# Kernel optimization log

Measured on AMD Instinct MI355X. Metric: run time of the kernel, lower is better.

## Reference

```python
import jax, jax.numpy as jnp
import numpy as np
from jax import lax

B, T, E, D, A, C, FILT = 32, 1600, 1024, 1024, 512, 10, 100
SCALING = 2.0


def setup_inputs() -> dict:
    key = jax.random.key(0)
    ks = jax.random.split(key, 14)
    enc_hs_pad = jax.random.normal(ks[0], (B, T, E), dtype=jnp.float32)
    # lengths in [T//2, T] so every row has valid positions
    enc_hs_len = jax.random.randint(ks[1], (B,), T // 2, T + 1, dtype=jnp.int32)
    dec_z = jax.random.normal(ks[2], (B, D), dtype=jnp.float32)
    # previous attention weights: uniform over valid frames, normalized
    valid = (jnp.arange(T)[None, :] < enc_hs_len[:, None]).astype(jnp.float32)
    raw = jax.random.uniform(ks[3], (B, T), dtype=jnp.float32) * valid
    att_prev = raw / jnp.sum(raw, axis=1, keepdims=True)
    att_h = 0.1 * jax.random.normal(ks[4], (B, A), dtype=jnp.float32)
    att_c = 0.1 * jax.random.normal(ks[5], (B, A), dtype=jnp.float32)
    W_enc = jax.random.normal(ks[6], (A, E), dtype=jnp.float32) / np.sqrt(E)
    b_enc = jax.random.normal(ks[7], (A,), dtype=jnp.float32) * 0.01
    W_dec = jax.random.normal(ks[8], (A, D), dtype=jnp.float32) / np.sqrt(D)
    conv_w = jax.random.normal(ks[9], (C, 1, 2 * FILT + 1), dtype=jnp.float32) / np.sqrt(2 * FILT + 1)
    W_ih = jax.random.normal(ks[10], (4 * A, C), dtype=jnp.float32) / np.sqrt(C)
    W_hh = jax.random.normal(ks[11], (4 * A, A), dtype=jnp.float32) / np.sqrt(A)
    W_g = jax.random.normal(ks[12], (A,), dtype=jnp.float32) / np.sqrt(A)
    b_g = jnp.zeros((1,), dtype=jnp.float32)
    return {"enc_hs_pad": enc_hs_pad, "enc_hs_len": enc_hs_len, "dec_z": dec_z,
            "att_prev": att_prev, "att_h": att_h, "att_c": att_c,
            "W_enc": W_enc, "b_enc": b_enc, "W_dec": W_dec, "conv_w": conv_w,
            "W_ih": W_ih, "W_hh": W_hh, "W_g": W_g, "b_g": b_g}


def reference(enc_hs_pad, enc_hs_len, dec_z, att_prev, att_h, att_c,
              W_enc, b_enc, W_dec, conv_w, W_ih, W_hh, W_g, b_g):
    t_len = enc_hs_pad.shape[1]
    filts = (conv_w.shape[-1] - 1) // 2

    # precompute encoder projection (B, T, A)
    pre_enc = jnp.einsum('bte,ae->bta', enc_hs_pad, W_enc) + b_enc

    # location conv on previous attention: (B,1,T) -> (B,C,T), relu, global max-pool over T
    att_conv = lax.conv_general_dilated(att_prev[:, None, :], conv_w,
                                        window_strides=(1,), padding=[(filts, filts)],
                                        dimension_numbers=('NCH', 'OIH', 'NCH'))
    att_feat = jnp.max(jax.nn.relu(att_conv), axis=-1)  # (B, C)

    # LSTMCell (no bias), pytorch gate order i, f, g, o
    gates = att_feat @ W_ih.T + att_h @ W_hh.T  # (B, 4A)
    i, f, g, o = jnp.split(gates, 4, axis=-1)
    c_new = jax.nn.sigmoid(f) * att_c + jax.nn.sigmoid(i) * jnp.tanh(g)
    h_new = jax.nn.sigmoid(o) * jnp.tanh(c_new)  # (B, A)

    dec_proj = dec_z @ W_dec.T  # (B, A)
    # scores (B, T)
    e = jnp.tanh(h_new[:, None, :] + pre_enc + dec_proj[:, None, :]) @ W_g + b_g

    mask = jnp.arange(t_len)[None, :] >= enc_hs_len[:, None]  # True = pad
    e = jnp.where(mask, jnp.finfo(e.dtype).min, e)
    w = jax.nn.softmax(SCALING * e, axis=1)  # (B, T)

    ctx = jnp.einsum('bt,bte->be', w, enc_hs_pad)  # (B, E)
    return ctx, w, h_new, c_new
```

## Files before the change

### kernel.cpp

```cpp
#include <hip/hip_runtime.h>

#define BB 32
#define TT 1600
#define EE 1024
#define DD 1024
#define AA 512
#define CC 10
#define KW 201

typedef __attribute__((ext_vector_type(8))) short short8;
typedef __attribute__((ext_vector_type(4))) float f32x4;

__device__ __forceinline__ unsigned short f2bf(float f) {
    unsigned int u = __float_as_uint(f);
    unsigned int r = (u + 0x7fffu + ((u >> 16) & 1u)) >> 16;
    return (unsigned short)r;
}
__device__ __forceinline__ float sigm(float x) { return 1.f / (1.f + expf(-x)); }

#define AF_OFF    0
#define GATES_OFF 320
#define DEC_OFF   65856
#define R_OFF     82240
#define E_OFF     98624
#define WBF_OFF   149824

#define CTX_OFF 0
#define W_OFF   32768
#define H_OFF   83968
#define C_OFF   100352

__global__ void zero_kernel(float* out, float* af) {
    int i = blockIdx.x * 256 + threadIdx.x;
    if (i < 32768) out[CTX_OFF + i] = 0.f;
    else if (i < 32768 + 320) af[i - 32768] = 0.f;
}

__global__ void wconv_kernel(const float* __restrict__ W_enc, unsigned short* __restrict__ Wbf) {
    int i = blockIdx.x * 256 + threadIdx.x;
    float4 v = reinterpret_cast<const float4*>(W_enc)[i];
    ushort4 p;
    p.x = f2bf(v.x); p.y = f2bf(v.y); p.z = f2bf(v.z); p.w = f2bf(v.w);
    reinterpret_cast<ushort4*>(Wbf)[i] = p;
}

__global__ void conv_kernel(const float* __restrict__ att_prev,
                            const float* __restrict__ conv_w,
                            unsigned int* __restrict__ af) {
    int b = blockIdx.x, c = blockIdx.y, seg = blockIdx.z;
    int ts = seg * 400;
    __shared__ float x[600];
    __shared__ float red[256];
    int tid = threadIdx.x;
    const float* xp = att_prev + b * TT;
    for (int i = tid; i < 600; i += 256) {
        int g = ts - 100 + i;
        x[i] = (g >= 0 && g < TT) ? xp[g] : 0.f;
    }
    __syncthreads();
    const float* wrow = conv_w + c * KW;
    float mx = 0.f;
    for (int tt = tid; tt < 400; tt += 256) {
        float s = 0.f;
        #pragma unroll 4
        for (int k = 0; k < KW; ++k) s += wrow[k] * x[tt + k];
        mx = fmaxf(mx, s);
    }
    red[tid] = mx; __syncthreads();
    for (int s = 128; s > 0; s >>= 1) {
        if (tid < s) red[tid] = fmaxf(red[tid], red[tid + s]);
        __syncthreads();
    }
    if (tid == 0) atomicMax(&af[b * CC + c], __float_as_uint(red[0]));
}

__global__ void small_gemm_kernel(const float* __restrict__ af,
                                  const float* __restrict__ att_h,
                                  const float* __restrict__ dec_z,
                                  const float* __restrict__ W_ih,
                                  const float* __restrict__ W_hh,
                                  const float* __restrict__ W_dec,
                                  float* __restrict__ gates,
                                  float* __restrict__ dec_proj) {
    int tid = threadIdx.x;
    int b = tid & 31, jl = tid >> 5;
    int j = blockIdx.x * 8 + jl;
    if (j < 2048) {
        float s = 0.f;
        #pragma unroll
        for (int k = 0; k < 10; ++k) s += af[b * 10 + k] * W_ih[j * 10 + k];
        const float4* hh4 = reinterpret_cast<const float4*>(W_hh + (size_t)j * 512);
        const float4* h4  = reinterpret_cast<const float4*>(att_h + b * 512);
        #pragma unroll 4
        for (int k = 0; k < 128; ++k) {
            float4 a = h4[k], w = hh4[k];
            s += a.x * w.x + a.y * w.y + a.z * w.z + a.w * w.w;
        }
        gates[b * 2048 + j] = s;
    } else {
        int a = j - 2048;
        const float4* wd4 = reinterpret_cast<const float4*>(W_dec + (size_t)a * 1024);
        const float4* z4  = reinterpret_cast<const float4*>(dec_z + b * 1024);
        float s = 0.f;
        #pragma unroll 4
        for (int k = 0; k < 256; ++k) {
            float4 a4 = z4[k], w = wd4[k];
            s += a4.x * w.x + a4.y * w.y + a4.z * w.z + a4.w * w.w;
        }
        dec_proj[b * 512 + a] = s;
    }
}

__global__ void lstm_kernel(const float* __restrict__ gates,
                            const float* __restrict__ att_c,
                            const float* __restrict__ dec_proj,
                            float* __restrict__ out,
                            float* __restrict__ r) {
    int idx = blockIdx.x * 256 + threadIdx.x;
    int b = idx >> 9, a = idx & 511;
    const float* g = gates + b * 2048;
    float ig = g[a], fg = g[512 + a], gg = g[1024 + a], og = g[1536 + a];
    float cn = sigm(fg) * att_c[idx] + sigm(ig) * tanhf(gg);
    float hn = sigm(og) * tanhf(cn);
    out[H_OFF + idx] = hn;
    out[C_OFF + idx] = cn;
    r[idx] = hn + dec_proj[idx];
}

__global__ void __launch_bounds__(256, 2)
score_gemm_kernel(const float* __restrict__ enc,
                  const unsigned short* __restrict__ Wbf,
                  const float* __restrict__ b_enc,
                  const float* __restrict__ r_ws,
                  const float* __restrict__ W_g,
                  const float* __restrict__ b_g,
                  float* __restrict__ e_out) {
    __shared__ short As[64 * 40];
    __shared__ short Bs[512 * 40];
    __shared__ float e_sm[64];

    int tid = threadIdx.x;
    int lane = tid & 63, wv = tid >> 6;
    int col = lane & 15, quad = lane >> 4;
    int m0 = blockIdx.x * 64;
    int b = blockIdx.x / 25;

    if (tid < 64) e_sm[tid] = 0.f;

    f32x4 acc[4][8];
    #pragma unroll
    for (int mt = 0; mt < 4; ++mt)
        #pragma unroll
        for (int nt = 0; nt < 8; ++nt)
            acc[mt][nt] = (f32x4){0.f, 0.f, 0.f, 0.f};

    for (int k0 = 0; k0 < 1024; k0 += 32) {
        __syncthreads();
        #pragma unroll
        for (int s = 0; s < 2; ++s) {
            int i = tid + s * 256;
            int row = i >> 3, kq = i & 7;
            float4 v = *reinterpret_cast<const float4*>(
                enc + (size_t)(m0 + row) * 1024 + k0 + kq * 4);
            ushort4 p;
            p.x = f2bf(v.x); p.y = f2bf(v.y); p.z = f2bf(v.z); p.w = f2bf(v.w);
            *reinterpret_cast<ushort4*>(&As[row * 40 + kq * 4]) = p;
        }
        #pragma unroll
        for (int s = 0; s < 8; ++s) {
            int i = tid + s * 256;
            int row = i >> 2, ko = (i & 3) * 8;
            int4 v = *reinterpret_cast<const int4*>(Wbf + (size_t)row * 1024 + k0 + ko);
            *reinterpret_cast<int4*>(&Bs[row * 40 + ko]) = v;
        }
        __syncthreads();

        short8 a_frag[4];
        #pragma unroll
        for (int mt = 0; mt < 4; ++mt)
            a_frag[mt] = *reinterpret_cast<const short8*>(&As[(mt * 16 + col) * 40 + quad * 8]);
        #pragma unroll
        for (int nt = 0; nt < 8; ++nt) {
            short8 b_frag = *reinterpret_cast<const short8*>(
                &Bs[(wv * 128 + nt * 16 + col) * 40 + quad * 8]);
            #pragma unroll
            for (int mt = 0; mt < 4; ++mt)
                acc[mt][nt] = __builtin_amdgcn_mfma_f32_16x16x32_bf16(
                    a_frag[mt], b_frag, acc[mt][nt], 0, 0, 0);
        }
    }

    float bn[8], rn[8], wg[8];
    #pragma unroll
    for (int nt = 0; nt < 8; ++nt) {
        int n = wv * 128 + nt * 16 + col;
        bn[nt] = b_enc[n];
        rn[nt] = r_ws[b * 512 + n];
        wg[nt] = W_g[n];
    }
    #pragma unroll
    for (int mt = 0; mt < 4; ++mt) {
        #pragma unroll
        for (int reg = 0; reg < 4; ++reg) {
            float p = 0.f;
            #pragma unroll
            for (int nt = 0; nt < 8; ++nt)
                p += wg[nt] * tanhf(acc[mt][nt][reg] + bn[nt] + rn[nt]);
            p += __shfl_xor(p, 1);
            p += __shfl_xor(p, 2);
            p += __shfl_xor(p, 4);
            p += __shfl_xor(p, 8);
            if (col == 0) atomicAdd(&e_sm[mt * 16 + quad * 4 + reg], p);
        }
    }
    __syncthreads();
    if (tid < 64) e_out[m0 + tid] = e_sm[tid] + b_g[0];
}

__global__ void softmax_kernel(const float* __restrict__ e_ws,
                               const int* __restrict__ lens,
                               float* __restrict__ w_out) {
    int b = blockIdx.x, tid = threadIdx.x;
    int len = lens[b];
    const float* e = e_ws + b * TT;
    __shared__ float red[256];
    float mx = -3.4e38f;
    for (int t = tid; t < len; t += 256) mx = fmaxf(mx, e[t]);
    red[tid] = mx; __syncthreads();
    for (int s = 128; s > 0; s >>= 1) {
        if (tid < s) red[tid] = fmaxf(red[tid], red[tid + s]);
        __syncthreads();
    }
    mx = red[0]; __syncthreads();
    float sum = 0.f;
    for (int t = tid; t < len; t += 256) sum += expf(2.f * (e[t] - mx));
    red[tid] = sum; __syncthreads();
    for (int s = 128; s > 0; s >>= 1) {
        if (tid < s) red[tid] += red[tid + s];
        __syncthreads();
    }
    float inv = 1.f / red[0];
    for (int t = tid; t < TT; t += 256)
        w_out[b * TT + t] = (t < len) ? expf(2.f * (e[t] - mx)) * inv : 0.f;
}

__global__ void ctx_kernel(const float* __restrict__ enc,
                           const float* __restrict__ w,
                           float* __restrict__ ctx) {
    int b = blockIdx.x, seg = blockIdx.y;
    int t0 = seg * 200;
    const float* wrow = w + b * TT;
    float4 acc = {0.f, 0.f, 0.f, 0.f};
    for (int t = t0; t < t0 + 200; ++t) {
        float wv = wrow[t];
        if (wv == 0.f) continue;
        float4 v = *reinterpret_cast<const float4*>(
            enc + (size_t)(b * TT + t) * 1024 + threadIdx.x * 4);
        acc.x += wv * v.x; acc.y += wv * v.y; acc.z += wv * v.z; acc.w += wv * v.w;
    }
    float* dst = ctx + b * 1024 + threadIdx.x * 4;
    atomicAdd(dst + 0, acc.x);
    atomicAdd(dst + 1, acc.y);
    atomicAdd(dst + 2, acc.z);
    atomicAdd(dst + 3, acc.w);
}

extern "C" void kernel_launch(void* const* d_in, const int* in_sizes, int n_in,
                              void* d_out, int out_size, void* d_ws, size_t ws_size,
                              hipStream_t stream) {
    const float* enc      = (const float*)d_in[0];
    const int*   lens     = (const int*)d_in[1];
    const float* dec_z    = (const float*)d_in[2];
    const float* att_prev = (const float*)d_in[3];
    const float* att_h    = (const float*)d_in[4];
    const float* att_c    = (const float*)d_in[5];
    const float* W_enc    = (const float*)d_in[6];
    const float* b_enc    = (const float*)d_in[7];
    const float* W_dec    = (const float*)d_in[8];
    const float* conv_w   = (const float*)d_in[9];
    const float* W_ih     = (const float*)d_in[10];
    const float* W_hh     = (const float*)d_in[11];
    const float* W_g      = (const float*)d_in[12];
    const float* b_g      = (const float*)d_in[13];

    float* out = (float*)d_out;
    float* ws  = (float*)d_ws;
    float* af        = ws + AF_OFF;
    float* gates     = ws + GATES_OFF;
    float* dec_proj  = ws + DEC_OFF;
    float* r_ws      = ws + R_OFF;
    float* e_ws      = ws + E_OFF;
    unsigned short* Wbf = (unsigned short*)(ws + WBF_OFF);

    zero_kernel<<<130, 256, 0, stream>>>(out, af);
    wconv_kernel<<<512, 256, 0, stream>>>(W_enc, Wbf);
    conv_kernel<<<dim3(BB, CC, 4), 256, 0, stream>>>(att_prev, conv_w, (unsigned int*)af);
    small_gemm_kernel<<<320, 256, 0, stream>>>(af, att_h, dec_z, W_ih, W_hh, W_dec,
                                               gates, dec_proj);
    lstm_kernel<<<64, 256, 0, stream>>>(gates, att_c, dec_proj, out, r_ws);
    score_gemm_kernel<<<800, 256, 0, stream>>>(enc, Wbf, b_enc, r_ws, W_g, b_g, e_ws);
    softmax_kernel<<<BB, 256, 0, stream>>>(e_ws, lens, out + W_OFF);
    ctx_kernel<<<dim3(BB, 8), 256, 0, stream>>>(enc, out + W_OFF, out + CTX_OFF);
}
```

Baseline: 559.3 us.

## Retile score GEMM to 128x128 blocks with direct-to-LDS weight loads

```diff
diff --git a/kernel.cpp b/kernel.cpp
--- a/kernel.cpp
+++ b/kernel.cpp
@@ -1,9 +1,9 @@
 #include <hip/hip_runtime.h>
+#include <hip/hip_bf16.h>
 
 #define BB 32
 #define TT 1600
 #define EE 1024
-#define DD 1024
 #define AA 512
 #define CC 10
 #define KW 201
@@ -11,12 +11,21 @@
 typedef __attribute__((ext_vector_type(8))) short short8;
 typedef __attribute__((ext_vector_type(4))) float f32x4;
 
-__device__ __forceinline__ unsigned short f2bf(float f) {
-    unsigned int u = __float_as_uint(f);
-    unsigned int r = (u + 0x7fffu + ((u >> 16) & 1u)) >> 16;
-    return (unsigned short)r;
-}
 __device__ __forceinline__ float sigm(float x) { return 1.f / (1.f + expf(-x)); }
+
+__device__ __forceinline__ unsigned int cvt2(float a, float b) {
+    float2 f2; f2.x = a; f2.y = b;
+    __hip_bfloat162 h = __float22bfloat162_rn(f2);
+    unsigned int r;
+    __builtin_memcpy(&r, &h, 4);
+    return r;
+}
+
+__device__ __forceinline__ void gl_lds16(const void* g, void* l) {
+    __builtin_amdgcn_global_load_lds(
+        (const __attribute__((address_space(1))) unsigned int*)g,
+        (__attribute__((address_space(3))) unsigned int*)l, 16, 0, 0);
+}
 
 #define AF_OFF    0
 #define GATES_OFF 320
@@ -30,18 +39,20 @@
 #define H_OFF   83968
 #define C_OFF   100352
 
-__global__ void zero_kernel(float* out, float* af) {
+__global__ void zero_kernel(float* out, float* af, float* e_ws) {
     int i = blockIdx.x * 256 + threadIdx.x;
     if (i < 32768) out[CTX_OFF + i] = 0.f;
-    else if (i < 32768 + 320) af[i - 32768] = 0.f;
+    else if (i < 33088) af[i - 32768] = 0.f;
+    else if (i < 84288) e_ws[i - 33088] = 0.f;
 }
 
 __global__ void wconv_kernel(const float* __restrict__ W_enc, unsigned short* __restrict__ Wbf) {
     int i = blockIdx.x * 256 + threadIdx.x;
     float4 v = reinterpret_cast<const float4*>(W_enc)[i];
-    ushort4 p;
-    p.x = f2bf(v.x); p.y = f2bf(v.y); p.z = f2bf(v.z); p.w = f2bf(v.w);
-    reinterpret_cast<ushort4*>(Wbf)[i] = p;
+    uint2 p;
+    p.x = cvt2(v.x, v.y);
+    p.y = cvt2(v.z, v.w);
+    reinterpret_cast<uint2*>(Wbf)[i] = p;
 }
 
 __global__ void conv_kernel(const float* __restrict__ att_prev,
@@ -50,6 +61,7 @@
     int b = blockIdx.x, c = blockIdx.y, seg = blockIdx.z;
     int ts = seg * 400;
     __shared__ float x[600];
+    __shared__ float wsm[KW];
     __shared__ float red[256];
     int tid = threadIdx.x;
     const float* xp = att_prev + b * TT;
@@ -57,13 +69,13 @@
         int g = ts - 100 + i;
         x[i] = (g >= 0 && g < TT) ? xp[g] : 0.f;
     }
+    if (tid < KW) wsm[tid] = conv_w[c * KW + tid];
     __syncthreads();
-    const float* wrow = conv_w + c * KW;
     float mx = 0.f;
     for (int tt = tid; tt < 400; tt += 256) {
         float s = 0.f;
         #pragma unroll 4
-        for (int k = 0; k < KW; ++k) s += wrow[k] * x[tt + k];
+        for (int k = 0; k < KW; ++k) s += wsm[k] * x[tt + k];
         mx = fmaxf(mx, s);
     }
     red[tid] = mx; __syncthreads();
@@ -133,56 +145,58 @@
                   const float* __restrict__ b_enc,
                   const float* __restrict__ r_ws,
                   const float* __restrict__ W_g,
-                  const float* __restrict__ b_g,
-                  float* __restrict__ e_out) {
-    __shared__ short As[64 * 40];
-    __shared__ short Bs[512 * 40];
-    __shared__ float e_sm[64];
+                  float* __restrict__ e_ws) {
+    __shared__ __align__(16) short As[128 * 32];
+    __shared__ __align__(16) short Bs[128 * 32];
 
     int tid = threadIdx.x;
     int lane = tid & 63, wv = tid >> 6;
     int col = lane & 15, quad = lane >> 4;
-    int m0 = blockIdx.x * 64;
-    int b = blockIdx.x / 25;
-
-    if (tid < 64) e_sm[tid] = 0.f;
-
-    f32x4 acc[4][8];
+    int wm = wv >> 1, wn = wv & 1;
+    int n0 = blockIdx.x * 128;
+    int m0 = blockIdx.y * 128;
+
+    int arow = tid >> 1, ahalf = (tid & 1) * 16;
+    const float* abase = enc + (size_t)(m0 + arow) * EE + ahalf;
+
+    f32x4 acc[4][4];
     #pragma unroll
     for (int mt = 0; mt < 4; ++mt)
         #pragma unroll
-        for (int nt = 0; nt < 8; ++nt)
+        for (int nt = 0; nt < 4; ++nt)
             acc[mt][nt] = (f32x4){0.f, 0.f, 0.f, 0.f};
 
-    for (int k0 = 0; k0 < 1024; k0 += 32) {
-        __syncthreads();
-        #pragma unroll
-        for (int s = 0; s < 2; ++s) {
-            int i = tid + s * 256;
-            int row = i >> 3, kq = i & 7;
-            float4 v = *reinterpret_cast<const float4*>(
-                enc + (size_t)(m0 + row) * 1024 + k0 + kq * 4);
-            ushort4 p;
-            p.x = f2bf(v.x); p.y = f2bf(v.y); p.z = f2bf(v.z); p.w = f2bf(v.w);
-            *reinterpret_cast<ushort4*>(&As[row * 40 + kq * 4]) = p;
-        }
-        #pragma unroll
-        for (int s = 0; s < 8; ++s) {
-            int i = tid + s * 256;
-            int row = i >> 2, ko = (i & 3) * 8;
-            int4 v = *reinterpret_cast<const int4*>(Wbf + (size_t)row * 1024 + k0 + ko);
-            *reinterpret_cast<int4*>(&Bs[row * 40 + ko]) = v;
-        }
+    for (int k0 = 0; k0 < EE; k0 += 32) {
+        const float4* ag = reinterpret_cast<const float4*>(abase + k0);
+        float4 v0 = ag[0], v1 = ag[1], v2 = ag[2], v3 = ag[3];
+
+        __syncthreads();
+
+        {
+            int c = tid;
+            gl_lds16(Wbf + (size_t)(n0 + (c >> 2)) * EE + k0 + (c & 3) * 8, Bs + c * 8);
+            c = tid + 256;
+            gl_lds16(Wbf + (size_t)(n0 + (c >> 2)) * EE + k0 + (c & 3) * 8, Bs + c * 8);
+        }
+        int4 st0, st1;
+        st0.x = cvt2(v0.x, v0.y); st0.y = cvt2(v0.z, v0.w);
+        st0.z = cvt2(v1.x, v1.y); st0.w = cvt2(v1.z, v1.w);
+        st1.x = cvt2(v2.x, v2.y); st1.y = cvt2(v2.z, v2.w);
+        st1.z = cvt2(v3.x, v3.y); st1.w = cvt2(v3.z, v3.w);
+        *reinterpret_cast<int4*>(&As[arow * 32 + ahalf]) = st0;
+        *reinterpret_cast<int4*>(&As[arow * 32 + ahalf + 8]) = st1;
+
         __syncthreads();
 
         short8 a_frag[4];
         #pragma unroll
         for (int mt = 0; mt < 4; ++mt)
-            a_frag[mt] = *reinterpret_cast<const short8*>(&As[(mt * 16 + col) * 40 + quad * 8]);
-        #pragma unroll
-        for (int nt = 0; nt < 8; ++nt) {
+            a_frag[mt] = *reinterpret_cast<const short8*>(
+                &As[(wm * 64 + mt * 16 + col) * 32 + quad * 8]);
+        #pragma unroll
+        for (int nt = 0; nt < 4; ++nt) {
             short8 b_frag = *reinterpret_cast<const short8*>(
-                &Bs[(wv * 128 + nt * 16 + col) * 40 + quad * 8]);
+                &Bs[(wn * 64 + nt * 16 + col) * 32 + quad * 8]);
             #pragma unroll
             for (int mt = 0; mt < 4; ++mt)
                 acc[mt][nt] = __builtin_amdgcn_mfma_f32_16x16x32_bf16(
@@ -190,31 +204,35 @@
         }
     }
 
-    float bn[8], rn[8], wg[8];
+    int n_base = n0 + wn * 64;
+    float wg[4], bn[4];
     #pragma unroll
-    for (int nt = 0; nt < 8; ++nt) {
-        int n = wv * 128 + nt * 16 + col;
+    for (int nt = 0; nt < 4; ++nt) {
+        int n = n_base + nt * 16 + col;
+        wg[nt] = W_g[n];
         bn[nt] = b_enc[n];
-        rn[nt] = r_ws[b * 512 + n];
-        wg[nt] = W_g[n];
     }
     #pragma unroll
     for (int mt = 0; mt < 4; ++mt) {
+        int mg = m0 + wm * 64 + mt * 16;
+        int bb = mg / TT;
+        float rn[4];
+        #pragma unroll
+        for (int nt = 0; nt < 4; ++nt)
+            rn[nt] = r_ws[bb * AA + n_base + nt * 16 + col];
         #pragma unroll
         for (int reg = 0; reg < 4; ++reg) {
             float p = 0.f;
             #pragma unroll
-            for (int nt = 0; nt < 8; ++nt)
+            for (int nt = 0; nt < 4; ++nt)
                 p += wg[nt] * tanhf(acc[mt][nt][reg] + bn[nt] + rn[nt]);
             p += __shfl_xor(p, 1);
             p += __shfl_xor(p, 2);
             p += __shfl_xor(p, 4);
             p += __shfl_xor(p, 8);
-            if (col == 0) atomicAdd(&e_sm[mt * 16 + quad * 4 + reg], p);
-        }
-    }
-    __syncthreads();
-    if (tid < 64) e_out[m0 + tid] = e_sm[tid] + b_g[0];
+            if (col == 0) atomicAdd(&e_ws[mg + quad * 4 + reg], p);
+        }
+    }
 }
 
 __global__ void softmax_kernel(const float* __restrict__ e_ws,
@@ -248,17 +266,23 @@
                            const float* __restrict__ w,
                            float* __restrict__ ctx) {
     int b = blockIdx.x, seg = blockIdx.y;
-    int t0 = seg * 200;
-    const float* wrow = w + b * TT;
+    int t0 = seg * 100;
+    const float* wrow = w + b * TT + t0;
+    const float* base = enc + ((size_t)(b * TT + t0)) * EE + threadIdx.x * 4;
     float4 acc = {0.f, 0.f, 0.f, 0.f};
-    for (int t = t0; t < t0 + 200; ++t) {
-        float wv = wrow[t];
-        if (wv == 0.f) continue;
-        float4 v = *reinterpret_cast<const float4*>(
-            enc + (size_t)(b * TT + t) * 1024 + threadIdx.x * 4);
-        acc.x += wv * v.x; acc.y += wv * v.y; acc.z += wv * v.z; acc.w += wv * v.w;
-    }
-    float* dst = ctx + b * 1024 + threadIdx.x * 4;
+    #pragma unroll 1
+    for (int i = 0; i < 100; i += 4) {
+        float w0 = wrow[i], w1 = wrow[i + 1], w2 = wrow[i + 2], w3 = wrow[i + 3];
+        float4 v0 = *reinterpret_cast<const float4*>(base + (size_t)(i + 0) * EE);
+        float4 v1 = *reinterpret_cast<const float4*>(base + (size_t)(i + 1) * EE);
+        float4 v2 = *reinterpret_cast<const float4*>(base + (size_t)(i + 2) * EE);
+        float4 v3 = *reinterpret_cast<const float4*>(base + (size_t)(i + 3) * EE);
+        acc.x += w0 * v0.x + w1 * v1.x + w2 * v2.x + w3 * v3.x;
+        acc.y += w0 * v0.y + w1 * v1.y + w2 * v2.y + w3 * v3.y;
+        acc.z += w0 * v0.z + w1 * v1.z + w2 * v2.z + w3 * v3.z;
+        acc.w += w0 * v0.w + w1 * v1.w + w2 * v2.w + w3 * v3.w;
+    }
+    float* dst = ctx + b * EE + threadIdx.x * 4;
     atomicAdd(dst + 0, acc.x);
     atomicAdd(dst + 1, acc.y);
     atomicAdd(dst + 2, acc.z);
@@ -281,7 +305,6 @@
     const float* W_ih     = (const float*)d_in[10];
     const float* W_hh     = (const float*)d_in[11];
     const float* W_g      = (const float*)d_in[12];
-    const float* b_g      = (const float*)d_in[13];
 
     float* out = (float*)d_out;
     float* ws  = (float*)d_ws;
@@ -292,13 +315,13 @@
     float* e_ws      = ws + E_OFF;
     unsigned short* Wbf = (unsigned short*)(ws + WBF_OFF);
 
-    zero_kernel<<<130, 256, 0, stream>>>(out, af);
+    zero_kernel<<<330, 256, 0, stream>>>(out, af, e_ws);
     wconv_kernel<<<512, 256, 0, stream>>>(W_enc, Wbf);
     conv_kernel<<<dim3(BB, CC, 4), 256, 0, stream>>>(att_prev, conv_w, (unsigned int*)af);
     small_gemm_kernel<<<320, 256, 0, stream>>>(af, att_h, dec_z, W_ih, W_hh, W_dec,
                                                gates, dec_proj);
     lstm_kernel<<<64, 256, 0, stream>>>(gates, att_c, dec_proj, out, r_ws);
-    score_gemm_kernel<<<800, 256, 0, stream>>>(enc, Wbf, b_enc, r_ws, W_g, b_g, e_ws);
+    score_gemm_kernel<<<dim3(4, 400), 256, 0, stream>>>(enc, Wbf, b_enc, r_ws, W_g, e_ws);
     softmax_kernel<<<BB, 256, 0, stream>>>(e_ws, lens, out + W_OFF);
-    ctx_kernel<<<dim3(BB, 8), 256, 0, stream>>>(enc, out + W_OFF, out + CTX_OFF);
-}
+    ctx_kernel<<<dim3(BB, 16), 256, 0, stream>>>(enc, out + W_OFF, out + CTX_OFF);
+}
```

Measured after the change: 524.8 us. -6.2%, faster.
